# Optimization experiments

Hardware: AMD Instinct MI355X
Metric: run time of the kernel (lower is better)

The kernel has to match this reference:

```python
import jax, jax.numpy as jnp
import numpy as np

H = W = 2048        # voxel grid
P0 = 0.1            # occupancy density
EPS = 1e-5          # BatchNorm eps (torch default)


def _grid(rs, cs):
    g = np.full((H, W), -1, np.int64)
    g[rs, cs] = np.arange(rs.size)
    return g


def _conv_map(g, rs, cs, s):
    # kernel map for 3x3 conv at tensor stride s: offsets {-s,0,s}^2, -1 = missing neighbor
    maps = []
    for dr in (-s, 0, s):
        for dc in (-s, 0, s):
            r2, c2 = rs + dr, cs + dc
            ok = (r2 >= 0) & (r2 < H) & (c2 >= 0) & (c2 < W)
            m = np.full(rs.size, -1, np.int64)
            m[ok] = g[r2[ok], c2[ok]]
            maps.append(m)
    return np.stack(maps, 1)  # [N, 9]


def _pool_map(g, rs, cs, s):
    # 2x2 max pool stride 2 at tensor stride s: out coords = floor to multiples of 2s
    out = np.unique(np.stack([rs - rs % (2 * s), cs - cs % (2 * s)], 1), axis=0)
    maps = []
    for dr in (0, s):
        for dc in (0, s):
            r2, c2 = out[:, 0] + dr, out[:, 1] + dc
            ok = (r2 < H) & (c2 < W)
            m = np.full(out.shape[0], -1, np.int64)
            m[ok] = g[r2[ok], c2[ok]]
            maps.append(m)
    return out, np.stack(maps, 1)  # coords, [N_out, 4]


def _build_maps():
    rng = np.random.default_rng(0)
    n0 = int(H * W * P0)
    flat = rng.choice(H * W, size=n0, replace=False)
    flat.sort()
    rs0, cs0 = np.divmod(flat, W)
    g0 = _grid(rs0, cs0)
    nbr0 = _conv_map(g0, rs0, cs0, 1)
    c1, pmap1 = _pool_map(g0, rs0, cs0, 1)
    g1 = _grid(c1[:, 0], c1[:, 1])
    nbr1 = _conv_map(g1, c1[:, 0], c1[:, 1], 2)
    c2, pmap2 = _pool_map(g1, c1[:, 0], c1[:, 1], 2)
    return n0, nbr0, pmap1, nbr1, pmap2, c2.shape[0]


def setup_inputs() -> dict:
    n0, nbr0, pmap1, nbr1, pmap2, n2 = _build_maps()
    key = jax.random.key(0)
    k0, k1, k2, k3 = jax.random.split(key, 4)
    f0 = jax.random.normal(k0, (n0, 1), jnp.float32)
    W1 = jax.random.normal(k1, (9, 1, 8), jnp.float32) * 0.3
    W2 = jax.random.normal(k2, (9, 8, 16), jnp.float32) * 0.12
    Wfc = jax.random.normal(k3, (16, 2), jnp.float32) * 0.25
    return dict(
        f0=f0, W1=W1, b1=jnp.zeros((8,), jnp.float32),
        gamma1=jnp.ones((8,), jnp.float32), beta1=jnp.zeros((8,), jnp.float32),
        W2=W2, b2=jnp.zeros((16,), jnp.float32),
        gamma2=jnp.ones((16,), jnp.float32), beta2=jnp.zeros((16,), jnp.float32),
        Wfc=Wfc, bfc=jnp.zeros((2,), jnp.float32),
        nbr0=jnp.asarray(nbr0), pmap1=jnp.asarray(pmap1),
        nbr1=jnp.asarray(nbr1), pmap2=jnp.asarray(pmap2),
    )


def _sparse_conv(f, nbr, Wk, b):
    # gather-matmul-scatter: missing neighbors contribute zero
    n = f.shape[0]
    fpad = jnp.concatenate([f, jnp.zeros((1, f.shape[1]), f.dtype)], 0)
    g = fpad[jnp.where(nbr < 0, n, nbr)]  # [N_out, 9, C_in]
    return jnp.einsum('nkc,kcd->nd', g, Wk) + b


def _bn_relu(x, gamma, beta):
    mu = x.mean(0)
    var = x.var(0)  # biased, as torch BN normalization
    return jax.nn.relu((x - mu) * jax.lax.rsqrt(var + EPS) * gamma + beta)


def _max_pool(f, pmap):
    # max over existing children only (every output has >= 1 child)
    n = f.shape[0]
    fpad = jnp.concatenate([f, jnp.full((1, f.shape[1]), -jnp.inf, f.dtype)], 0)
    return fpad[jnp.where(pmap < 0, n, pmap)].max(1)


def reference(f0, W1, b1, gamma1, beta1, W2, b2, gamma2, beta2, Wfc, bfc,
              nbr0, pmap1, nbr1, pmap2):
    x = _bn_relu(_sparse_conv(f0, nbr0, W1, b1), gamma1, beta1)
    x = _max_pool(x, pmap1)
    x = _bn_relu(_sparse_conv(x, nbr1, W2, b2), gamma2, beta2)
    x = _max_pool(x, pmap2)
    return x @ Wfc + bfc
```

## Files before the change

### kernel.cpp

```cpp
#include <hip/hip_runtime.h>

#define EPS 1e-5f
#define NSLOT 64

__device__ __forceinline__ float waveReduceSum(float v) {
    #pragma unroll
    for (int off = 32; off > 0; off >>= 1)
        v += __shfl_down(v, off, 64);
    return v;
}

__global__ void k_conv1(const float* __restrict__ f0, const float* __restrict__ W1,
                        const float* __restrict__ b1, const int* __restrict__ nbr0,
                        float* __restrict__ x1, float* __restrict__ slots, int n0) {
    __shared__ float sW[72];
    __shared__ float sred[16];
    int t = threadIdx.x;
    if (t < 72) sW[t] = W1[t];
    if (t < 16) sred[t] = 0.f;
    __syncthreads();

    int n = blockIdx.x * blockDim.x + t;
    bool valid = (n < n0);
    float acc[8];
    if (valid) {
        #pragma unroll
        for (int c = 0; c < 8; ++c) acc[c] = b1[c];
        #pragma unroll
        for (int k = 0; k < 9; ++k) {
            int j = nbr0[(size_t)n * 9 + k];
            if (j >= 0) {
                float v = f0[j];
                #pragma unroll
                for (int c = 0; c < 8; ++c) acc[c] = fmaf(v, sW[k * 8 + c], acc[c]);
            }
        }
        float4 lo = {acc[0], acc[1], acc[2], acc[3]};
        float4 hi = {acc[4], acc[5], acc[6], acc[7]};
        float4* dst = (float4*)(x1 + (size_t)n * 8);
        dst[0] = lo; dst[1] = hi;
    } else {
        #pragma unroll
        for (int c = 0; c < 8; ++c) acc[c] = 0.f;
    }

    #pragma unroll
    for (int c = 0; c < 8; ++c) {
        float s = waveReduceSum(acc[c]);
        float q = waveReduceSum(acc[c] * acc[c]);
        if ((t & 63) == 0) {
            atomicAdd(&sred[c], s);
            atomicAdd(&sred[8 + c], q);
        }
    }
    __syncthreads();
    if (t < 16) {
        float* slot = slots + (size_t)(blockIdx.x & (NSLOT - 1)) * 64;
        atomicAdd(&slot[t], sred[t]);
    }
}

__global__ void k_finalize(const float* __restrict__ slots, float* __restrict__ stats,
                           int base, int cnt) {
    int c = threadIdx.x;
    if (c >= cnt) return;
    float s = 0.f;
    #pragma unroll 8
    for (int k = 0; k < NSLOT; ++k) s += slots[(size_t)k * 64 + base + c];
    stats[base + c] = s;
}

__global__ void k_pool1(const float* __restrict__ x1, const int* __restrict__ pmap1,
                        const float* __restrict__ stats, const float* __restrict__ gamma1,
                        const float* __restrict__ beta1, float* __restrict__ p1,
                        int n1, float invn) {
    int i = blockIdx.x * blockDim.x + threadIdx.x;
    if (i >= n1) return;
    float m[8], sc[8], bb[8];
    #pragma unroll
    for (int c = 0; c < 8; ++c) {
        float mu  = stats[c] * invn;
        float var = stats[8 + c] * invn - mu * mu;
        m[c]  = mu;
        sc[c] = rsqrtf(var + EPS) * gamma1[c];
        bb[c] = beta1[c];
    }
    float best[8];
    #pragma unroll
    for (int c = 0; c < 8; ++c) best[c] = 0.f;
    #pragma unroll
    for (int k = 0; k < 4; ++k) {
        int j = pmap1[(size_t)i * 4 + k];
        if (j >= 0) {
            const float4* src = (const float4*)(x1 + (size_t)j * 8);
            float4 lo = src[0], hi = src[1];
            float v[8] = {lo.x, lo.y, lo.z, lo.w, hi.x, hi.y, hi.z, hi.w};
            #pragma unroll
            for (int c = 0; c < 8; ++c) {
                float z = fmaxf(fmaf(v[c] - m[c], sc[c], bb[c]), 0.f);
                best[c] = fmaxf(best[c], z);
            }
        }
    }
    float4 lo = {best[0], best[1], best[2], best[3]};
    float4 hi = {best[4], best[5], best[6], best[7]};
    float4* dst = (float4*)(p1 + (size_t)i * 8);
    dst[0] = lo; dst[1] = hi;
}

__global__ void k_conv2(const float* __restrict__ p1, const float* __restrict__ W2,
                        const float* __restrict__ b2, const int* __restrict__ nbr1,
                        float* __restrict__ x2, float* __restrict__ slots, int n1) {
    __shared__ float sW[1152];
    __shared__ float sred[32];
    for (int t = threadIdx.x; t < 1152; t += blockDim.x) sW[t] = W2[t];
    if (threadIdx.x < 32) sred[threadIdx.x] = 0.f;
    __syncthreads();

    int n = blockIdx.x * blockDim.x + threadIdx.x;
    bool valid = (n < n1);
    float acc[16];
    if (valid) {
        #pragma unroll
        for (int c = 0; c < 16; ++c) acc[c] = b2[c];
        #pragma unroll
        for (int k = 0; k < 9; ++k) {
            int j = nbr1[(size_t)n * 9 + k];
            if (j >= 0) {
                const float4* src = (const float4*)(p1 + (size_t)j * 8);
                float4 lo = src[0], hi = src[1];
                float g[8] = {lo.x, lo.y, lo.z, lo.w, hi.x, hi.y, hi.z, hi.w};
                #pragma unroll
                for (int ci = 0; ci < 8; ++ci) {
                    const float* w = &sW[(k * 8 + ci) * 16];
                    #pragma unroll
                    for (int c = 0; c < 16; ++c) acc[c] = fmaf(g[ci], w[c], acc[c]);
                }
            }
        }
        float4* dst = (float4*)(x2 + (size_t)n * 16);
        #pragma unroll
        for (int q4 = 0; q4 < 4; ++q4) {
            float4 v = {acc[q4 * 4], acc[q4 * 4 + 1], acc[q4 * 4 + 2], acc[q4 * 4 + 3]};
            dst[q4] = v;
        }
    } else {
        #pragma unroll
        for (int c = 0; c < 16; ++c) acc[c] = 0.f;
    }

    #pragma unroll
    for (int c = 0; c < 16; ++c) {
        float s = waveReduceSum(acc[c]);
        float q = waveReduceSum(acc[c] * acc[c]);
        if ((threadIdx.x & 63) == 0) {
            atomicAdd(&sred[c], s);
            atomicAdd(&sred[16 + c], q);
        }
    }
    __syncthreads();
    if (threadIdx.x < 32) {
        float* slot = slots + (size_t)(blockIdx.x & (NSLOT - 1)) * 64;
        atomicAdd(&slot[16 + threadIdx.x], sred[threadIdx.x]);
    }
}

__global__ void k_pool2_fc(const float* __restrict__ x2, const int* __restrict__ pmap2,
                           const float* __restrict__ stats, const float* __restrict__ gamma2,
                           const float* __restrict__ beta2, const float* __restrict__ Wfc,
                           const float* __restrict__ bfc, float* __restrict__ out,
                           int n2, float invn) {
    int i = blockIdx.x * blockDim.x + threadIdx.x;
    if (i >= n2) return;
    float m[16], sc[16], bb[16];
    #pragma unroll
    for (int c = 0; c < 16; ++c) {
        float mu  = stats[16 + c] * invn;
        float var = stats[32 + c] * invn - mu * mu;
        m[c]  = mu;
        sc[c] = rsqrtf(var + EPS) * gamma2[c];
        bb[c] = beta2[c];
    }
    float best[16];
    #pragma unroll
    for (int c = 0; c < 16; ++c) best[c] = 0.f;
    #pragma unroll
    for (int k = 0; k < 4; ++k) {
        int j = pmap2[(size_t)i * 4 + k];
        if (j >= 0) {
            const float4* src = (const float4*)(x2 + (size_t)j * 16);
            #pragma unroll
            for (int q4 = 0; q4 < 4; ++q4) {
                float4 v4 = src[q4];
                float v[4] = {v4.x, v4.y, v4.z, v4.w};
                #pragma unroll
                for (int c = 0; c < 4; ++c) {
                    int cc = q4 * 4 + c;
                    float z = fmaxf(fmaf(v[c] - m[cc], sc[cc], bb[cc]), 0.f);
                    best[cc] = fmaxf(best[cc], z);
                }
            }
        }
    }
    float o0 = bfc[0], o1 = bfc[1];
    #pragma unroll
    for (int c = 0; c < 16; ++c) {
        o0 = fmaf(best[c], Wfc[c * 2 + 0], o0);
        o1 = fmaf(best[c], Wfc[c * 2 + 1], o1);
    }
    out[(size_t)i * 2 + 0] = o0;
    out[(size_t)i * 2 + 1] = o1;
}

extern "C" void kernel_launch(void* const* d_in, const int* in_sizes, int n_in,
                              void* d_out, int out_size, void* d_ws, size_t ws_size,
                              hipStream_t stream) {
    const float* f0     = (const float*)d_in[0];
    const float* W1     = (const float*)d_in[1];
    const float* b1     = (const float*)d_in[2];
    const float* gamma1 = (const float*)d_in[3];
    const float* beta1  = (const float*)d_in[4];
    const float* W2     = (const float*)d_in[5];
    const float* b2     = (const float*)d_in[6];
    const float* gamma2 = (const float*)d_in[7];
    const float* beta2  = (const float*)d_in[8];
    const float* Wfc    = (const float*)d_in[9];
    const float* bfc    = (const float*)d_in[10];
    const int*   nbr0   = (const int*)d_in[11];
    const int*   pmap1  = (const int*)d_in[12];
    const int*   nbr1   = (const int*)d_in[13];
    const int*   pmap2  = (const int*)d_in[14];

    const int n0 = in_sizes[0];
    const int n1 = in_sizes[12] / 4;
    const int n2 = in_sizes[14] / 4;

    float* ws    = (float*)d_ws;
    float* slots = ws;
    float* stats = ws + (size_t)NSLOT * 64;
    float* x1    = stats + 64;
    float* p1    = x1 + (size_t)n0 * 8;
    float* x2    = p1 + (size_t)n1 * 8;

    hipMemsetAsync(slots, 0, ((size_t)NSLOT * 64 + 64) * sizeof(float), stream);

    const int B = 256;
    k_conv1<<<(n0 + B - 1) / B, B, 0, stream>>>(f0, W1, b1, nbr0, x1, slots, n0);
    k_finalize<<<1, 64, 0, stream>>>(slots, stats, 0, 16);
    k_pool1<<<(n1 + B - 1) / B, B, 0, stream>>>(x1, pmap1, stats, gamma1, beta1, p1,
                                                n1, 1.0f / (float)n0);
    k_conv2<<<(n1 + B - 1) / B, B, 0, stream>>>(p1, W2, b2, nbr1, x2, slots, n1);
    k_finalize<<<1, 64, 0, stream>>>(slots, stats, 16, 32);
    k_pool2_fc<<<(n2 + B - 1) / B, B, 0, stream>>>(x2, pmap2, stats, gamma2, beta2,
                                                   Wfc, bfc, (float*)d_out,
                                                   n2, 1.0f / (float)n1);
}
```

Baseline: 87.99 us.

## Fuse BN stat finalize into pool kernels and batch neighbor gathers branch-free

Removes the two single-block finalize kernels: each pool block now reduces the 64 partial-sum slots itself with a wave reduction into shared memory. The conv and pool kernels load all neighbor indices up front and issue gathers unconditionally, clamping missing neighbors to index 0 and masking afterwards, so more loads are in flight at once. Pool maps are read as int4 and launch bounds are added. The cost is redundant slot reads in every pool block, extra registers, and wasted loads for missing neighbors.

New measurement: 119.3 us. +35.6%, slower.

```diff
diff --git a/kernel.cpp b/kernel.cpp
--- a/kernel.cpp
+++ b/kernel.cpp
@@ -10,9 +10,10 @@
     return v;
 }
 
-__global__ void k_conv1(const float* __restrict__ f0, const float* __restrict__ W1,
-                        const float* __restrict__ b1, const int* __restrict__ nbr0,
-                        float* __restrict__ x1, float* __restrict__ slots, int n0) {
+__global__ __launch_bounds__(256) void k_conv1(
+        const float* __restrict__ f0, const float* __restrict__ W1,
+        const float* __restrict__ b1, const int* __restrict__ nbr0,
+        float* __restrict__ x1, float* __restrict__ slots, int n0) {
     __shared__ float sW[72];
     __shared__ float sred[16];
     int t = threadIdx.x;
@@ -22,19 +23,27 @@
 
     int n = blockIdx.x * blockDim.x + t;
     bool valid = (n < n0);
+    int nn = valid ? n : (n0 - 1);
+
+    int idx[9];
+    #pragma unroll
+    for (int k = 0; k < 9; ++k) idx[k] = nbr0[(size_t)nn * 9 + k];
+    float v[9];
+    #pragma unroll
+    for (int k = 0; k < 9; ++k) {
+        float f = f0[idx[k] >= 0 ? idx[k] : 0];
+        v[k] = (idx[k] >= 0) ? f : 0.f;
+    }
+
     float acc[8];
+    #pragma unroll
+    for (int c = 0; c < 8; ++c) acc[c] = b1[c];
+    #pragma unroll
+    for (int k = 0; k < 9; ++k)
+        #pragma unroll
+        for (int c = 0; c < 8; ++c) acc[c] = fmaf(v[k], sW[k * 8 + c], acc[c]);
+
     if (valid) {
-        #pragma unroll
-        for (int c = 0; c < 8; ++c) acc[c] = b1[c];
-        #pragma unroll
-        for (int k = 0; k < 9; ++k) {
-            int j = nbr0[(size_t)n * 9 + k];
-            if (j >= 0) {
-                float v = f0[j];
-                #pragma unroll
-                for (int c = 0; c < 8; ++c) acc[c] = fmaf(v, sW[k * 8 + c], acc[c]);
-            }
-        }
         float4 lo = {acc[0], acc[1], acc[2], acc[3]};
         float4 hi = {acc[4], acc[5], acc[6], acc[7]};
         float4* dst = (float4*)(x1 + (size_t)n * 8);
@@ -60,46 +69,55 @@
     }
 }
 
-__global__ void k_finalize(const float* __restrict__ slots, float* __restrict__ stats,
-                           int base, int cnt) {
-    int c = threadIdx.x;
-    if (c >= cnt) return;
-    float s = 0.f;
-    #pragma unroll 8
-    for (int k = 0; k < NSLOT; ++k) s += slots[(size_t)k * 64 + base + c];
-    stats[base + c] = s;
-}
-
-__global__ void k_pool1(const float* __restrict__ x1, const int* __restrict__ pmap1,
-                        const float* __restrict__ stats, const float* __restrict__ gamma1,
-                        const float* __restrict__ beta1, float* __restrict__ p1,
-                        int n1, float invn) {
-    int i = blockIdx.x * blockDim.x + threadIdx.x;
+__global__ __launch_bounds__(256) void k_pool1(
+        const float* __restrict__ x1, const int* __restrict__ pmap1,
+        const float* __restrict__ slots, const float* __restrict__ gamma1,
+        const float* __restrict__ beta1, float* __restrict__ p1,
+        int n1, float invn) {
+    __shared__ float sstat[16];
+    int t = threadIdx.x;
+    if (t < 64) {
+        const float4* s4 = (const float4*)(slots + (size_t)t * 64);
+        float4 a = s4[0], b = s4[1], c4 = s4[2], d = s4[3];
+        float vals[16] = {a.x, a.y, a.z, a.w, b.x, b.y, b.z, b.w,
+                          c4.x, c4.y, c4.z, c4.w, d.x, d.y, d.z, d.w};
+        #pragma unroll
+        for (int c = 0; c < 16; ++c) {
+            float s = waveReduceSum(vals[c]);
+            if (t == 0) sstat[c] = s;
+        }
+    }
+    __syncthreads();
+
+    int i = blockIdx.x * blockDim.x + t;
     if (i >= n1) return;
+
     float m[8], sc[8], bb[8];
     #pragma unroll
     for (int c = 0; c < 8; ++c) {
-        float mu  = stats[c] * invn;
-        float var = stats[8 + c] * invn - mu * mu;
+        float mu  = sstat[c] * invn;
+        float var = sstat[8 + c] * invn - mu * mu;
         m[c]  = mu;
         sc[c] = rsqrtf(var + EPS) * gamma1[c];
         bb[c] = beta1[c];
     }
+
+    int4 pm = ((const int4*)pmap1)[i];
+    int idx[4] = {pm.x, pm.y, pm.z, pm.w};
     float best[8];
     #pragma unroll
     for (int c = 0; c < 8; ++c) best[c] = 0.f;
     #pragma unroll
     for (int k = 0; k < 4; ++k) {
-        int j = pmap1[(size_t)i * 4 + k];
-        if (j >= 0) {
-            const float4* src = (const float4*)(x1 + (size_t)j * 8);
-            float4 lo = src[0], hi = src[1];
-            float v[8] = {lo.x, lo.y, lo.z, lo.w, hi.x, hi.y, hi.z, hi.w};
-            #pragma unroll
-            for (int c = 0; c < 8; ++c) {
-                float z = fmaxf(fmaf(v[c] - m[c], sc[c], bb[c]), 0.f);
-                best[c] = fmaxf(best[c], z);
-            }
+        int j = idx[k] >= 0 ? idx[k] : 0;
+        const float4* src = (const float4*)(x1 + (size_t)j * 8);
+        float4 lo = src[0], hi = src[1];
+        float v[8] = {lo.x, lo.y, lo.z, lo.w, hi.x, hi.y, hi.z, hi.w};
+        #pragma unroll
+        for (int c = 0; c < 8; ++c) {
+            float z = fmaxf(fmaf(v[c] - m[c], sc[c], bb[c]), 0.f);
+            z = (idx[k] >= 0) ? z : 0.f;
+            best[c] = fmaxf(best[c], z);
         }
     }
     float4 lo = {best[0], best[1], best[2], best[3]};
@@ -108,9 +126,10 @@
     dst[0] = lo; dst[1] = hi;
 }
 
-__global__ void k_conv2(const float* __restrict__ p1, const float* __restrict__ W2,
-                        const float* __restrict__ b2, const int* __restrict__ nbr1,
-                        float* __restrict__ x2, float* __restrict__ slots, int n1) {
+__global__ __launch_bounds__(256) void k_conv2(
+        const float* __restrict__ p1, const float* __restrict__ W2,
+        const float* __restrict__ b2, const int* __restrict__ nbr1,
+        float* __restrict__ x2, float* __restrict__ slots, int n1) {
     __shared__ float sW[1152];
     __shared__ float sred[32];
     for (int t = threadIdx.x; t < 1152; t += blockDim.x) sW[t] = W2[t];
@@ -119,25 +138,41 @@
 
     int n = blockIdx.x * blockDim.x + threadIdx.x;
     bool valid = (n < n1);
+    int nn = valid ? n : (n1 - 1);
+
+    int idx[9];
+    #pragma unroll
+    for (int k = 0; k < 9; ++k) idx[k] = nbr1[(size_t)nn * 9 + k];
+
+    float4 glo[9], ghi[9];
+    #pragma unroll
+    for (int k = 0; k < 9; ++k) {
+        const float4* src = (const float4*)(p1 + (size_t)(idx[k] >= 0 ? idx[k] : 0) * 8);
+        glo[k] = src[0];
+        ghi[k] = src[1];
+    }
+    const float4 z4 = {0.f, 0.f, 0.f, 0.f};
+    #pragma unroll
+    for (int k = 0; k < 9; ++k) {
+        if (idx[k] < 0) { glo[k] = z4; ghi[k] = z4; }
+    }
+
     float acc[16];
+    #pragma unroll
+    for (int c = 0; c < 16; ++c) acc[c] = b2[c];
+    #pragma unroll
+    for (int k = 0; k < 9; ++k) {
+        float g[8] = {glo[k].x, glo[k].y, glo[k].z, glo[k].w,
+                      ghi[k].x, ghi[k].y, ghi[k].z, ghi[k].w};
+        #pragma unroll
+        for (int ci = 0; ci < 8; ++ci) {
+            const float* w = &sW[(k * 8 + ci) * 16];
+            #pragma unroll
+            for (int c = 0; c < 16; ++c) acc[c] = fmaf(g[ci], w[c], acc[c]);
+        }
+    }
+
     if (valid) {
-        #pragma unroll
-        for (int c = 0; c < 16; ++c) acc[c] = b2[c];
-        #pragma unroll
-        for (int k = 0; k < 9; ++k) {
-            int j = nbr1[(size_t)n * 9 + k];
-            if (j >= 0) {
-                const float4* src = (const float4*)(p1 + (size_t)j * 8);
-                float4 lo = src[0], hi = src[1];
-                float g[8] = {lo.x, lo.y, lo.z, lo.w, hi.x, hi.y, hi.z, hi.w};
-                #pragma unroll
-                for (int ci = 0; ci < 8; ++ci) {
-                    const float* w = &sW[(k * 8 + ci) * 16];
-                    #pragma unroll
-                    for (int c = 0; c < 16; ++c) acc[c] = fmaf(g[ci], w[c], acc[c]);
-                }
-            }
-        }
         float4* dst = (float4*)(x2 + (size_t)n * 16);
         #pragma unroll
         for (int q4 = 0; q4 < 4; ++q4) {
@@ -165,40 +200,63 @@
     }
 }
 
-__global__ void k_pool2_fc(const float* __restrict__ x2, const int* __restrict__ pmap2,
-                           const float* __restrict__ stats, const float* __restrict__ gamma2,
-                           const float* __restrict__ beta2, const float* __restrict__ Wfc,
-                           const float* __restrict__ bfc, float* __restrict__ out,
-                           int n2, float invn) {
-    int i = blockIdx.x * blockDim.x + threadIdx.x;
+__global__ __launch_bounds__(256) void k_pool2_fc(
+        const float* __restrict__ x2, const int* __restrict__ pmap2,
+        const float* __restrict__ slots, const float* __restrict__ gamma2,
+        const float* __restrict__ beta2, const float* __restrict__ Wfc,
+        const float* __restrict__ bfc, float* __restrict__ out,
+        int n2, float invn) {
+    __shared__ float sstat[32];
+    int t = threadIdx.x;
+    if (t < 64) {
+        const float4* s4 = (const float4*)(slots + (size_t)t * 64 + 16);
+        float vals[32];
+        #pragma unroll
+        for (int q = 0; q < 8; ++q) {
+            float4 a = s4[q];
+            vals[q * 4 + 0] = a.x; vals[q * 4 + 1] = a.y;
+            vals[q * 4 + 2] = a.z; vals[q * 4 + 3] = a.w;
+        }
+        #pragma unroll
+        for (int c = 0; c < 32; ++c) {
+            float s = waveReduceSum(vals[c]);
+            if (t == 0) sstat[c] = s;
+        }
+    }
+    __syncthreads();
+
+    int i = blockIdx.x * blockDim.x + t;
     if (i >= n2) return;
+
     float m[16], sc[16], bb[16];
     #pragma unroll
     for (int c = 0; c < 16; ++c) {
-        float mu  = stats[16 + c] * invn;
-        float var = stats[32 + c] * invn - mu * mu;
+        float mu  = sstat[c] * invn;
+        float var = sstat[16 + c] * invn - mu * mu;
         m[c]  = mu;
         sc[c] = rsqrtf(var + EPS) * gamma2[c];
         bb[c] = beta2[c];
     }
+
+    int4 pm = ((const int4*)pmap2)[i];
+    int idx[4] = {pm.x, pm.y, pm.z, pm.w};
     float best[16];
     #pragma unroll
     for (int c = 0; c < 16; ++c) best[c] = 0.f;
     #pragma unroll
     for (int k = 0; k < 4; ++k) {
-        int j = pmap2[(size_t)i * 4 + k];
-        if (j >= 0) {
-            const float4* src = (const float4*)(x2 + (size_t)j * 16);
+        int j = idx[k] >= 0 ? idx[k] : 0;
+        const float4* src = (const float4*)(x2 + (size_t)j * 16);
+        #pragma unroll
+        for (int q4 = 0; q4 < 4; ++q4) {
+            float4 v4 = src[q4];
+            float v[4] = {v4.x, v4.y, v4.z, v4.w};
             #pragma unroll
-            for (int q4 = 0; q4 < 4; ++q4) {
-                float4 v4 = src[q4];
-                float v[4] = {v4.x, v4.y, v4.z, v4.w};
-                #pragma unroll
-                for (int c = 0; c < 4; ++c) {
-                    int cc = q4 * 4 + c;
-                    float z = fmaxf(fmaf(v[c] - m[cc], sc[cc], bb[cc]), 0.f);
-                    best[cc] = fmaxf(best[cc], z);
-                }
+            for (int c = 0; c < 4; ++c) {
+                int cc = q4 * 4 + c;
+                float z = fmaxf(fmaf(v[c] - m[cc], sc[cc], bb[cc]), 0.f);
+                z = (idx[k] >= 0) ? z : 0.f;
+                best[cc] = fmaxf(best[cc], z);
             }
         }
     }
@@ -237,21 +295,18 @@
 
     float* ws    = (float*)d_ws;
     float* slots = ws;
-    float* stats = ws + (size_t)NSLOT * 64;
-    float* x1    = stats + 64;
+    float* x1    = ws + (size_t)NSLOT * 64;
     float* p1    = x1 + (size_t)n0 * 8;
     float* x2    = p1 + (size_t)n1 * 8;
 
-    hipMemsetAsync(slots, 0, ((size_t)NSLOT * 64 + 64) * sizeof(float), stream);
+    hipMemsetAsync(slots, 0, (size_t)NSLOT * 64 * sizeof(float), stream);
 
     const int B = 256;
     k_conv1<<<(n0 + B - 1) / B, B, 0, stream>>>(f0, W1, b1, nbr0, x1, slots, n0);
-    k_finalize<<<1, 64, 0, stream>>>(slots, stats, 0, 16);
-    k_pool1<<<(n1 + B - 1) / B, B, 0, stream>>>(x1, pmap1, stats, gamma1, beta1, p1,
+    k_pool1<<<(n1 + B - 1) / B, B, 0, stream>>>(x1, pmap1, slots, gamma1, beta1, p1,
                                                 n1, 1.0f / (float)n0);
     k_conv2<<<(n1 + B - 1) / B, B, 0, stream>>>(p1, W2, b2, nbr1, x2, slots, n1);
-    k_finalize<<<1, 64, 0, stream>>>(slots, stats, 16, 32);
-    k_pool2_fc<<<(n2 + B - 1) / B, B, 0, stream>>>(x2, pmap2, stats, gamma2, beta2,
+    k_pool2_fc<<<(n2 + B - 1) / B, B, 0, stream>>>(x2, pmap2, slots, gamma2, beta2,
                                                    Wfc, bfc, (float*)d_out,
                                                    n2, 1.0f / (float)n1);
 }
```
